# Kernel optimization log

Measured on AMD Instinct MI355X. Metric: run time of the kernel, lower is better.

The kernel has to match this reference:

```python
import jax, jax.numpy as jnp
import numpy as np

B = 64          # graphs per batch
N_NODES = 2000  # nodes per graph (model hyperparameter: FC2 in_features)
NF = 128        # node features
H = 8           # hidden_dim
OC = 8          # out_channels
NC = 2          # n_classes
DEG = 16        # avg degree
SLOPE = 0.01


def _lin_init(key, fan_in, fan_out):
    k1, k2 = jax.random.split(key)
    s = 1.0 / np.sqrt(fan_in)
    W = jax.random.uniform(k1, (fan_in, fan_out), jnp.float32, -s, s)
    b = jax.random.uniform(k2, (fan_out,), jnp.float32, -s, s)
    return W, b


def setup_inputs() -> dict:
    key = jax.random.key(0)
    ks = jax.random.split(key, 10)
    N = B * N_NODES
    E = N * DEG
    x = jax.random.normal(ks[0], (N, NF), jnp.float32)
    # graph-local random edges, offset per graph
    local = jax.random.randint(ks[1], (2, E), 0, N_NODES)
    off = jnp.repeat(jnp.arange(B, dtype=jnp.int64) * N_NODES, E // B)
    edge_index = (local + off[None, :]).astype(jnp.int64)
    batch = jnp.repeat(jnp.arange(B, dtype=jnp.int64), N_NODES)
    W1a, b1a = _lin_init(ks[2], NF, H)
    W1b, b1b = _lin_init(ks[3], H, H)
    W2a, b2a = _lin_init(ks[4], H, H)
    W2b, b2b = _lin_init(ks[5], H, OC)
    Wf1, bf1 = _lin_init(ks[6], OC, 1)
    Wf2, bf2 = _lin_init(ks[7], N_NODES, NC)
    return {"x": x, "edge_index": edge_index, "batch": batch,
            "W1a": W1a, "b1a": b1a, "W1b": W1b, "b1b": b1b,
            "W2a": W2a, "b2a": b2a, "W2b": W2b, "b2b": b2b,
            "Wf1": Wf1, "bf1": bf1, "Wf2": Wf2, "bf2": bf2}


def _lrelu(v):
    return jnp.where(v >= 0, v, SLOPE * v)


def _gin_conv(h, src, dst, Wa, ba, Wb, bb):
    N = h.shape[0]
    agg = jax.ops.segment_sum(h[src], dst, num_segments=N)  # sum_{j->i} h_j
    z = h + agg                                             # (1+eps)*h + agg, eps=0
    z = _lrelu(z @ Wa + ba)                                 # MLP linear1 + act
    return z @ Wb + bb                                      # MLP linear2 (plain last)


def reference(x, edge_index, batch, W1a, b1a, W1b, b1b, W2a, b2a, W2b, b2b,
              Wf1, bf1, Wf2, bf2):
    src, dst = edge_index[0], edge_index[1]
    h = _gin_conv(x, src, dst, W1a, b1a, W1b, b1b)
    h = _lrelu(h)  # inter-layer activation (dropout = identity at eval)
    h = _gin_conv(h, src, dst, W2a, b2a, W2b, b2b)  # [N, OC], no act after last conv
    bsz = h.shape[0] // N_NODES
    y = h.reshape(bsz, N_NODES, OC)
    y = _lrelu(y) @ Wf1 + bf1          # FC1 -> [B, n_nodes, 1]
    y = y.reshape(bsz, N_NODES)
    y = _lrelu(y) @ Wf2 + bf2          # FC2 -> [B, n_classes]
    return jax.nn.log_softmax(y, axis=1)
```

## Files before the change

### kernel.cpp

```cpp
#include <hip/hip_runtime.h>
#include <math.h>

#define NF 128
#define HD 8
#define NPG 2000
#define EPB 8000
#define NPB 500
#define FNPB 128
#define SLOPE 0.01f

__device__ __forceinline__ float lrelu(float v) {
    return v > 0.0f ? v : SLOPE * v;
}
__device__ __forceinline__ unsigned short f2bf(float f) {
    unsigned int u = __float_as_uint(f);
    return (unsigned short)((u + 0x7FFFu + ((u >> 16) & 1u)) >> 16);
}
__device__ __forceinline__ float bfl(unsigned int p) {
    return __uint_as_float(p << 16);
}
__device__ __forceinline__ float bfh(unsigned int p) {
    return __uint_as_float(p & 0xFFFF0000u);
}

__global__ __launch_bounds__(1024) void k_featsort(
    const float* __restrict__ x, const float* __restrict__ W1a,
    const int* __restrict__ ei, unsigned short* __restrict__ t1b,
    unsigned short* __restrict__ gcolb, int* __restrict__ rpc,
    int N, int E, int NC)
{
    __shared__ union {
        struct { float tile[FNPB * 132]; float wl[NF * HD]; } f;
        struct { int cnt[NPG]; int srt[EPB]; int wtot[16]; int wpre[16]; } s;
    } sm;

    const int tid = threadIdx.x;

    if ((int)blockIdx.x < NC) {
        const int b = blockIdx.x;
        const int g = b >> 2;
        const int lane = tid & 63;
        const int wv = tid >> 6;
        const int nodeBase = g * NPG;
        const int e0 = b * EPB;

        for (int i = tid; i < NPG; i += 1024) sm.s.cnt[i] = 0;
        __syncthreads();

        for (int e = e0 + tid; e < e0 + EPB; e += 1024) {
            int dl = ei[E + e] - nodeBase;
            atomicAdd(&sm.s.cnt[dl], 1);
        }
        __syncthreads();

        int c0 = 0, c1 = 0;
        if (tid < 1000) { c0 = sm.s.cnt[2 * tid]; c1 = sm.s.cnt[2 * tid + 1]; }
        int s = c0 + c1;
        int isc = s;
#pragma unroll
        for (int d = 1; d < 64; d <<= 1) {
            int o = __shfl_up(isc, d);
            if (lane >= d) isc += o;
        }
        if (lane == 63) sm.s.wtot[wv] = isc;
        __syncthreads();
        if (wv == 0) {
            int v = (lane < 16) ? sm.s.wtot[lane] : 0;
            int iv = v;
#pragma unroll
            for (int d = 1; d < 16; d <<= 1) {
                int o = __shfl_up(iv, d);
                if (lane >= d) iv += o;
            }
            if (lane < 16) sm.s.wpre[lane] = iv - v;
        }
        __syncthreads();
        int excl = isc - s + sm.s.wpre[wv];

        int* rpb = rpc + (size_t)b * (NPG + 1);
        if (tid < 1000) {
            sm.s.cnt[2 * tid]     = excl;
            sm.s.cnt[2 * tid + 1] = excl + c0;
            rpb[2 * tid]     = excl;
            rpb[2 * tid + 1] = excl + c0;
        }
        if (tid == 0) rpb[NPG] = EPB;
        __syncthreads();

        for (int e = e0 + tid; e < e0 + EPB; e += 1024) {
            int src = ei[e] - nodeBase;
            int dl = ei[E + e] - nodeBase;
            int pos = atomicAdd(&sm.s.cnt[dl], 1);
            sm.s.srt[pos] = src;
        }
        __syncthreads();

        unsigned int* dst = (unsigned int*)(gcolb + (size_t)b * EPB);
        for (int i = tid; i < EPB / 2; i += 1024) {
            unsigned int lo = (unsigned int)sm.s.srt[2 * i] & 0xFFFFu;
            unsigned int hi = (unsigned int)sm.s.srt[2 * i + 1] << 16;
            dst[i] = lo | hi;
        }
    } else {
        const size_t base = (size_t)(blockIdx.x - NC) * FNPB;

        if (tid < 256) ((float4*)sm.f.wl)[tid] = ((const float4*)W1a)[tid];

        const float4* xg = (const float4*)(x + base * NF);
#pragma unroll
        for (int i = 0; i < 4; ++i) {
            int idx = tid + i * 1024;
            float4 v = xg[idx];
            int n = idx >> 5;
            int k4 = idx & 31;
            *(float4*)(sm.f.tile + n * 132 + k4 * 4) = v;
        }
        __syncthreads();

        const int n = tid >> 3;
        const int col = tid & 7;
        float acc = 0.0f;
        const float* row = sm.f.tile + n * 132;
#pragma unroll
        for (int k4 = 0; k4 < 32; ++k4) {
            float4 r = *(const float4*)(row + k4 * 4);
            int kb = k4 * 4 * HD + col;
            acc += r.x * sm.f.wl[kb];
            acc += r.y * sm.f.wl[kb + HD];
            acc += r.z * sm.f.wl[kb + 2 * HD];
            acc += r.w * sm.f.wl[kb + 3 * HD];
        }
        t1b[(base + n) * HD + col] = f2bf(acc);
    }
}

#define GATHER_CHUNK(P)                                                       \
    {                                                                         \
        int b0 = rs[P], cnt = re[P] - b0;                                     \
        int sl[8];                                                            \
        _Pragma("unroll")                                                     \
        for (int j = 0; j < 8; ++j) {                                         \
            int idx = (j < cnt) ? (b0 + j) : 0;                \
            sl[j] = colp[P][idx];                                             \
        }                                                                     \
        _Pragma("unroll")                                                     \
        for (int j = 0; j < 8; ++j) {                                         \
            float w = (j < cnt) ? 1.0f : 0.0f;                                \
            uint4 v = tbl[sl[j]];                                             \
            a0 += w * bfl(v.x); a1 += w * bfh(v.x);                           \
            a2 += w * bfl(v.y); a3 += w * bfh(v.y);                           \
            a4 += w * bfl(v.z); a5 += w * bfh(v.z);                           \
            a6 += w * bfl(v.w); a7 += w * bfh(v.w);                           \
        }                                                                     \
        for (int e2 = b0 + 8; e2 < b0 + cnt; ++e2) {           \
            uint4 v = tbl[colp[P][e2]];                                       \
            a0 += bfl(v.x); a1 += bfh(v.x);                                   \
            a2 += bfl(v.y); a3 += bfh(v.y);                                   \
            a4 += bfl(v.z); a5 += bfh(v.z);                                   \
            a6 += bfl(v.w); a7 += bfh(v.w);                                   \
        }                                                                     \
    }

__global__ __launch_bounds__(512) void k_l1(
    const unsigned short* __restrict__ t1b, const int* __restrict__ rpc,
    const unsigned short* __restrict__ gcolb, unsigned short* __restrict__ ub,
    const float* __restrict__ b1a, const float* __restrict__ W1b,
    const float* __restrict__ b1b, const float* __restrict__ W2a)
{
    __shared__ uint4 tbl[NPG];
    __shared__ float wts[144];

    const int b = blockIdx.x;
    const int g = b >> 2;
    const int q = b & 3;
    const int tid = threadIdx.x;

    if (tid < 144) {
        float v;
        if (tid < 8)       v = b1a[tid];
        else if (tid < 72) v = W1b[tid - 8];
        else if (tid < 80) v = b1b[tid - 72];
        else               v = W2a[tid - 80];
        wts[tid] = v;
    }

    const uint4* src4 = (const uint4*)(t1b + (size_t)g * NPG * HD);
#pragma unroll
    for (int i = 0; i < 4; ++i) {
        int idx = tid + i * 512;
        if (idx < NPG) tbl[idx] = src4[idx];
    }
    __syncthreads();

    if (tid < NPB) {
        const int nl = q * NPB + tid;
        int rs[4], re[4];
        const unsigned short* colp[4];
#pragma unroll
        for (int p = 0; p < 4; ++p) {
            const int* rpb = rpc + (size_t)((g << 2) + p) * (NPG + 1);
            colp[p] = gcolb + (size_t)((g << 2) + p) * EPB;
            rs[p] = rpb[nl]; re[p] = rpb[nl + 1];
        }
        float a0 = 0, a1 = 0, a2 = 0, a3 = 0, a4 = 0, a5 = 0, a6 = 0, a7 = 0;
        GATHER_CHUNK(0) GATHER_CHUNK(1) GATHER_CHUNK(2) GATHER_CHUNK(3)

        uint4 sv = tbl[nl];
        float z[HD];
        z[0] = lrelu(bfl(sv.x) + a0 + wts[0]); z[1] = lrelu(bfh(sv.x) + a1 + wts[1]);
        z[2] = lrelu(bfl(sv.y) + a2 + wts[2]); z[3] = lrelu(bfh(sv.y) + a3 + wts[3]);
        z[4] = lrelu(bfl(sv.z) + a4 + wts[4]); z[5] = lrelu(bfh(sv.z) + a5 + wts[5]);
        z[6] = lrelu(bfl(sv.w) + a6 + wts[6]); z[7] = lrelu(bfh(sv.w) + a7 + wts[7]);

        float h[HD];
#pragma unroll
        for (int j = 0; j < HD; ++j) {
            float acc = wts[72 + j];
#pragma unroll
            for (int c = 0; c < HD; ++c) acc += z[c] * wts[8 + c * HD + j];
            h[j] = lrelu(acc);
        }
        float uu[HD];
#pragma unroll
        for (int j = 0; j < HD; ++j) {
            float acc = 0.0f;
#pragma unroll
            for (int c = 0; c < HD; ++c) acc += h[c] * wts[80 + c * HD + j];
            uu[j] = acc;
        }
        uint4 pk;
        pk.x = (unsigned int)f2bf(uu[0]) | ((unsigned int)f2bf(uu[1]) << 16);
        pk.y = (unsigned int)f2bf(uu[2]) | ((unsigned int)f2bf(uu[3]) << 16);
        pk.z = (unsigned int)f2bf(uu[4]) | ((unsigned int)f2bf(uu[5]) << 16);
        pk.w = (unsigned int)f2bf(uu[6]) | ((unsigned int)f2bf(uu[7]) << 16);
        ((uint4*)ub)[(size_t)g * NPG + nl] = pk;
    }
}

__global__ __launch_bounds__(512) void k_l2(
    const unsigned short* __restrict__ ub, const int* __restrict__ rpc,
    const unsigned short* __restrict__ gcolb,
    const float* __restrict__ b2a, const float* __restrict__ W2b,
    const float* __restrict__ b2b, const float* __restrict__ Wf1,
    const float* __restrict__ bf1, const float* __restrict__ Wf2,
    float* __restrict__ bparts)
{
    __shared__ uint4 tbl[NPG];
    __shared__ float wts[89];
    __shared__ float red[16];

    const int b = blockIdx.x;
    const int g = b >> 2;
    const int q = b & 3;
    const int tid = threadIdx.x;
    const int lane = tid & 63;
    const int wv = tid >> 6;

    if (tid < 89) {
        float v;
        if (tid < 8)       v = b2a[tid];
        else if (tid < 72) v = W2b[tid - 8];
        else if (tid < 80) v = b2b[tid - 72];
        else if (tid < 88) v = Wf1[tid - 80];
        else               v = bf1[0];
        wts[tid] = v;
    }

    const uint4* src4 = (const uint4*)(ub + (size_t)g * NPG * HD);
#pragma unroll
    for (int i = 0; i < 4; ++i) {
        int idx = tid + i * 512;
        if (idx < NPG) tbl[idx] = src4[idx];
    }
    __syncthreads();

    float acc0 = 0.0f, acc1 = 0.0f;
    if (tid < NPB) {
        const int nl = q * NPB + tid;
        int rs[4], re[4];
        const unsigned short* colp[4];
#pragma unroll
        for (int p = 0; p < 4; ++p) {
            const int* rpb = rpc + (size_t)((g << 2) + p) * (NPG + 1);
            colp[p] = gcolb + (size_t)((g << 2) + p) * EPB;
            rs[p] = rpb[nl]; re[p] = rpb[nl + 1];
        }
        float a0 = 0, a1 = 0, a2 = 0, a3 = 0, a4 = 0, a5 = 0, a6 = 0, a7 = 0;
        GATHER_CHUNK(0) GATHER_CHUNK(1) GATHER_CHUNK(2) GATHER_CHUNK(3)

        uint4 sv = tbl[nl];
        float z[HD];
        z[0] = lrelu(bfl(sv.x) + a0 + wts[0]); z[1] = lrelu(bfh(sv.x) + a1 + wts[1]);
        z[2] = lrelu(bfl(sv.y) + a2 + wts[2]); z[3] = lrelu(bfh(sv.y) + a3 + wts[3]);
        z[4] = lrelu(bfl(sv.z) + a4 + wts[4]); z[5] = lrelu(bfh(sv.z) + a5 + wts[5]);
        z[6] = lrelu(bfl(sv.w) + a6 + wts[6]); z[7] = lrelu(bfh(sv.w) + a7 + wts[7]);

        float svl = wts[88];
#pragma unroll
        for (int j = 0; j < HD; ++j) {
            float acc = wts[72 + j];
#pragma unroll
            for (int c = 0; c < HD; ++c) acc += z[c] * wts[8 + c * HD + j];
            svl += lrelu(acc) * wts[80 + j];
        }
        float pf = lrelu(svl);
        float2 wf = *(const float2*)(Wf2 + (size_t)nl * 2);
        acc0 = pf * wf.x;
        acc1 = pf * wf.y;
    }

#pragma unroll
    for (int off = 32; off > 0; off >>= 1) {
        acc0 += __shfl_down(acc0, off);
        acc1 += __shfl_down(acc1, off);
    }
    if (lane == 0) { red[wv * 2] = acc0; red[wv * 2 + 1] = acc1; }
    __syncthreads();

    if (tid == 0) {
        float y0 = 0.f, y1 = 0.f;
#pragma unroll
        for (int w = 0; w < 8; ++w) { y0 += red[w * 2]; y1 += red[w * 2 + 1]; }
        *(float2*)(bparts + (size_t)b * 2) = make_float2(y0, y1);
    }
}

__global__ __launch_bounds__(64) void k_fin(const float* __restrict__ bparts,
                                            const float* __restrict__ bf2,
                                            float* __restrict__ out, int Bn) {
    int g = threadIdx.x;
    if (g >= Bn) return;
    float y0 = bf2[0], y1 = bf2[1];
#pragma unroll
    for (int b = 0; b < 4; ++b) {
        float2 v = *(const float2*)(bparts + (size_t)(g * 4 + b) * 2);
        y0 += v.x; y1 += v.y;
    }
    float m = fmaxf(y0, y1);
    float lse = m + logf(expf(y0 - m) + expf(y1 - m));
    out[g * 2 + 0] = y0 - lse;
    out[g * 2 + 1] = y1 - lse;
}

extern "C" void kernel_launch(void* const* d_in, const int* in_sizes, int n_in,
                              void* d_out, int out_size, void* d_ws, size_t ws_size,
                              hipStream_t stream) {
    const float* x   = (const float*)d_in[0];
    const int*   ei  = (const int*)  d_in[1];
    const float* W1a = (const float*)d_in[3];
    const float* b1a = (const float*)d_in[4];
    const float* W1b = (const float*)d_in[5];
    const float* b1b = (const float*)d_in[6];
    const float* W2a = (const float*)d_in[7];
    const float* b2a = (const float*)d_in[8];
    const float* W2b = (const float*)d_in[9];
    const float* b2b = (const float*)d_in[10];
    const float* Wf1 = (const float*)d_in[11];
    const float* bf1 = (const float*)d_in[12];
    const float* Wf2 = (const float*)d_in[13];
    const float* bf2 = (const float*)d_in[14];

    int N   = in_sizes[0] / NF;
    int E   = in_sizes[1] / 2;
    int Bn  = N / NPG;
    int NC  = Bn * 4;

    unsigned short* t1b   = (unsigned short*)d_ws;
    unsigned short* ubuf  = t1b + (size_t)N * HD;
    unsigned short* gcolb = ubuf + (size_t)N * HD;
    int*            rpc   = (int*)(gcolb + (size_t)E);
    float*          bparts= (float*)(rpc + (size_t)NC * (NPG + 1) + 16);

    k_featsort<<<NC + N / FNPB, 1024, 0, stream>>>(x, W1a, ei, t1b, gcolb, rpc,
                                                   N, E, NC);
    k_l1 <<<NC, 512, 0, stream>>>(t1b, rpc, gcolb, ubuf, b1a, W1b, b1b, W2a);
    k_l2 <<<NC, 512, 0, stream>>>(ubuf, rpc, gcolb, b2a, W2b, b2b, Wf1, bf1,
                                  Wf2, bparts);
    k_fin<<<1, 64, 0, stream>>>(bparts, bf2, (float*)d_out, Bn);
}
```

Before: 154.4 us.

## Split node gathers across thread pairs and cache packed edges in LDS

The layer kernels now launch 8 blocks per graph and assign two threads per node, each summing two of the four edge chunks before an xor-shuffle combine; only one thread of each pair runs the MLP. The sort phase stores packed (dst,src) pairs in shared memory during counting so the scatter pass avoids rereading edge_index from global memory. The aim is more parallelism and shorter per-thread serial gather chains. In exchange, each block reloads the per-graph node table twice as often in total, and LDS use grows in the sort branch.

```diff
diff --git a/kernel.cpp b/kernel.cpp
--- a/kernel.cpp
+++ b/kernel.cpp
@@ -5,7 +5,8 @@
 #define HD 8
 #define NPG 2000
 #define EPB 8000
-#define NPB 500
+#define LPB 8
+#define LNPB 250
 #define FNPB 128
 #define SLOPE 0.01f
 
@@ -31,7 +32,8 @@
 {
     __shared__ union {
         struct { float tile[FNPB * 132]; float wl[NF * HD]; } f;
-        struct { int cnt[NPG]; int srt[EPB]; int wtot[16]; int wpre[16]; } s;
+        struct { int cnt[NPG]; unsigned int pck[EPB]; int srt[EPB];
+                 int wtot[16]; int wpre[16]; } s;
     } sm;
 
     const int tid = threadIdx.x;
@@ -48,7 +50,9 @@
         __syncthreads();
 
         for (int e = e0 + tid; e < e0 + EPB; e += 1024) {
+            int src = ei[e] - nodeBase;
             int dl = ei[E + e] - nodeBase;
+            sm.s.pck[e - e0] = ((unsigned int)dl << 11) | (unsigned int)src;
             atomicAdd(&sm.s.cnt[dl], 1);
         }
         __syncthreads();
@@ -87,9 +91,10 @@
         if (tid == 0) rpb[NPG] = EPB;
         __syncthreads();
 
-        for (int e = e0 + tid; e < e0 + EPB; e += 1024) {
-            int src = ei[e] - nodeBase;
-            int dl = ei[E + e] - nodeBase;
+        for (int i = tid; i < EPB; i += 1024) {
+            unsigned int p = sm.s.pck[i];
+            int dl = (int)(p >> 11);
+            int src = (int)(p & 2047u);
             int pos = atomicAdd(&sm.s.cnt[dl], 1);
             sm.s.srt[pos] = src;
         }
@@ -140,7 +145,7 @@
         int sl[8];                                                            \
         _Pragma("unroll")                                                     \
         for (int j = 0; j < 8; ++j) {                                         \
-            int idx = (j < cnt) ? (b0 + j) : 0;                \
+            int idx = (j < cnt) ? (b0 + j) : 0;                               \
             sl[j] = colp[P][idx];                                             \
         }                                                                     \
         _Pragma("unroll")                                                     \
@@ -152,7 +157,7 @@
             a4 += w * bfl(v.z); a5 += w * bfh(v.z);                           \
             a6 += w * bfl(v.w); a7 += w * bfh(v.w);                           \
         }                                                                     \
-        for (int e2 = b0 + 8; e2 < b0 + cnt; ++e2) {           \
+        for (int e2 = b0 + 8; e2 < b0 + cnt; ++e2) {                          \
             uint4 v = tbl[colp[P][e2]];                                       \
             a0 += bfl(v.x); a1 += bfh(v.x);                                   \
             a2 += bfl(v.y); a3 += bfh(v.y);                                   \
@@ -171,8 +176,8 @@
     __shared__ float wts[144];
 
     const int b = blockIdx.x;
-    const int g = b >> 2;
-    const int q = b & 3;
+    const int g = b >> 3;
+    const int q = b & 7;
     const int tid = threadIdx.x;
 
     if (tid < 144) {
@@ -192,48 +197,57 @@
     }
     __syncthreads();
 
-    if (tid < NPB) {
-        const int nl = q * NPB + tid;
-        int rs[4], re[4];
-        const unsigned short* colp[4];
-#pragma unroll
-        for (int p = 0; p < 4; ++p) {
-            const int* rpb = rpc + (size_t)((g << 2) + p) * (NPG + 1);
-            colp[p] = gcolb + (size_t)((g << 2) + p) * EPB;
+    if (tid < 2 * LNPB) {
+        const int node = tid >> 1;
+        const int half = tid & 1;
+        const int nl = q * LNPB + node;
+        int rs[2], re[2];
+        const unsigned short* colp[2];
+#pragma unroll
+        for (int p = 0; p < 2; ++p) {
+            int ch = half * 2 + p;
+            const int* rpb = rpc + (size_t)((g << 2) + ch) * (NPG + 1);
+            colp[p] = gcolb + (size_t)((g << 2) + ch) * EPB;
             rs[p] = rpb[nl]; re[p] = rpb[nl + 1];
         }
         float a0 = 0, a1 = 0, a2 = 0, a3 = 0, a4 = 0, a5 = 0, a6 = 0, a7 = 0;
-        GATHER_CHUNK(0) GATHER_CHUNK(1) GATHER_CHUNK(2) GATHER_CHUNK(3)
-
-        uint4 sv = tbl[nl];
-        float z[HD];
-        z[0] = lrelu(bfl(sv.x) + a0 + wts[0]); z[1] = lrelu(bfh(sv.x) + a1 + wts[1]);
-        z[2] = lrelu(bfl(sv.y) + a2 + wts[2]); z[3] = lrelu(bfh(sv.y) + a3 + wts[3]);
-        z[4] = lrelu(bfl(sv.z) + a4 + wts[4]); z[5] = lrelu(bfh(sv.z) + a5 + wts[5]);
-        z[6] = lrelu(bfl(sv.w) + a6 + wts[6]); z[7] = lrelu(bfh(sv.w) + a7 + wts[7]);
-
-        float h[HD];
-#pragma unroll
-        for (int j = 0; j < HD; ++j) {
-            float acc = wts[72 + j];
-#pragma unroll
-            for (int c = 0; c < HD; ++c) acc += z[c] * wts[8 + c * HD + j];
-            h[j] = lrelu(acc);
-        }
-        float uu[HD];
-#pragma unroll
-        for (int j = 0; j < HD; ++j) {
-            float acc = 0.0f;
-#pragma unroll
-            for (int c = 0; c < HD; ++c) acc += h[c] * wts[80 + c * HD + j];
-            uu[j] = acc;
-        }
-        uint4 pk;
-        pk.x = (unsigned int)f2bf(uu[0]) | ((unsigned int)f2bf(uu[1]) << 16);
-        pk.y = (unsigned int)f2bf(uu[2]) | ((unsigned int)f2bf(uu[3]) << 16);
-        pk.z = (unsigned int)f2bf(uu[4]) | ((unsigned int)f2bf(uu[5]) << 16);
-        pk.w = (unsigned int)f2bf(uu[6]) | ((unsigned int)f2bf(uu[7]) << 16);
-        ((uint4*)ub)[(size_t)g * NPG + nl] = pk;
+        GATHER_CHUNK(0) GATHER_CHUNK(1)
+        a0 += __shfl_xor(a0, 1); a1 += __shfl_xor(a1, 1);
+        a2 += __shfl_xor(a2, 1); a3 += __shfl_xor(a3, 1);
+        a4 += __shfl_xor(a4, 1); a5 += __shfl_xor(a5, 1);
+        a6 += __shfl_xor(a6, 1); a7 += __shfl_xor(a7, 1);
+
+        if (half == 0) {
+            uint4 sv = tbl[nl];
+            float z[HD];
+            z[0] = lrelu(bfl(sv.x) + a0 + wts[0]); z[1] = lrelu(bfh(sv.x) + a1 + wts[1]);
+            z[2] = lrelu(bfl(sv.y) + a2 + wts[2]); z[3] = lrelu(bfh(sv.y) + a3 + wts[3]);
+            z[4] = lrelu(bfl(sv.z) + a4 + wts[4]); z[5] = lrelu(bfh(sv.z) + a5 + wts[5]);
+            z[6] = lrelu(bfl(sv.w) + a6 + wts[6]); z[7] = lrelu(bfh(sv.w) + a7 + wts[7]);
+
+            float h[HD];
+#pragma unroll
+            for (int j = 0; j < HD; ++j) {
+                float acc = wts[72 + j];
+#pragma unroll
+                for (int c = 0; c < HD; ++c) acc += z[c] * wts[8 + c * HD + j];
+                h[j] = lrelu(acc);
+            }
+            float uu[HD];
+#pragma unroll
+            for (int j = 0; j < HD; ++j) {
+                float acc = 0.0f;
+#pragma unroll
+                for (int c = 0; c < HD; ++c) acc += h[c] * wts[80 + c * HD + j];
+                uu[j] = acc;
+            }
+            uint4 pk;
+            pk.x = (unsigned int)f2bf(uu[0]) | ((unsigned int)f2bf(uu[1]) << 16);
+            pk.y = (unsigned int)f2bf(uu[2]) | ((unsigned int)f2bf(uu[3]) << 16);
+            pk.z = (unsigned int)f2bf(uu[4]) | ((unsigned int)f2bf(uu[5]) << 16);
+            pk.w = (unsigned int)f2bf(uu[6]) | ((unsigned int)f2bf(uu[7]) << 16);
+            ((uint4*)ub)[(size_t)g * NPG + nl] = pk;
+        }
     }
 }
 
@@ -250,8 +264,8 @@
     __shared__ float red[16];
 
     const int b = blockIdx.x;
-    const int g = b >> 2;
-    const int q = b & 3;
+    const int g = b >> 3;
+    const int q = b & 7;
     const int tid = threadIdx.x;
     const int lane = tid & 63;
     const int wv = tid >> 6;
@@ -275,38 +289,47 @@
     __syncthreads();
 
     float acc0 = 0.0f, acc1 = 0.0f;
-    if (tid < NPB) {
-        const int nl = q * NPB + tid;
-        int rs[4], re[4];
-        const unsigned short* colp[4];
-#pragma unroll
-        for (int p = 0; p < 4; ++p) {
-            const int* rpb = rpc + (size_t)((g << 2) + p) * (NPG + 1);
-            colp[p] = gcolb + (size_t)((g << 2) + p) * EPB;
+    if (tid < 2 * LNPB) {
+        const int node = tid >> 1;
+        const int half = tid & 1;
+        const int nl = q * LNPB + node;
+        int rs[2], re[2];
+        const unsigned short* colp[2];
+#pragma unroll
+        for (int p = 0; p < 2; ++p) {
+            int ch = half * 2 + p;
+            const int* rpb = rpc + (size_t)((g << 2) + ch) * (NPG + 1);
+            colp[p] = gcolb + (size_t)((g << 2) + ch) * EPB;
             rs[p] = rpb[nl]; re[p] = rpb[nl + 1];
         }
         float a0 = 0, a1 = 0, a2 = 0, a3 = 0, a4 = 0, a5 = 0, a6 = 0, a7 = 0;
-        GATHER_CHUNK(0) GATHER_CHUNK(1) GATHER_CHUNK(2) GATHER_CHUNK(3)
-
-        uint4 sv = tbl[nl];
-        float z[HD];
-        z[0] = lrelu(bfl(sv.x) + a0 + wts[0]); z[1] = lrelu(bfh(sv.x) + a1 + wts[1]);
-        z[2] = lrelu(bfl(sv.y) + a2 + wts[2]); z[3] = lrelu(bfh(sv.y) + a3 + wts[3]);
-        z[4] = lrelu(bfl(sv.z) + a4 + wts[4]); z[5] = lrelu(bfh(sv.z) + a5 + wts[5]);
-        z[6] = lrelu(bfl(sv.w) + a6 + wts[6]); z[7] = lrelu(bfh(sv.w) + a7 + wts[7]);
-
-        float svl = wts[88];
-#pragma unroll
-        for (int j = 0; j < HD; ++j) {
-            float acc = wts[72 + j];
-#pragma unroll
-            for (int c = 0; c < HD; ++c) acc += z[c] * wts[8 + c * HD + j];
-            svl += lrelu(acc) * wts[80 + j];
-        }
-        float pf = lrelu(svl);
-        float2 wf = *(const float2*)(Wf2 + (size_t)nl * 2);
-        acc0 = pf * wf.x;
-        acc1 = pf * wf.y;
+        GATHER_CHUNK(0) GATHER_CHUNK(1)
+        a0 += __shfl_xor(a0, 1); a1 += __shfl_xor(a1, 1);
+        a2 += __shfl_xor(a2, 1); a3 += __shfl_xor(a3, 1);
+        a4 += __shfl_xor(a4, 1); a5 += __shfl_xor(a5, 1);
+        a6 += __shfl_xor(a6, 1); a7 += __shfl_xor(a7, 1);
+
+        if (half == 0) {
+            uint4 sv = tbl[nl];
+            float z[HD];
+            z[0] = lrelu(bfl(sv.x) + a0 + wts[0]); z[1] = lrelu(bfh(sv.x) + a1 + wts[1]);
+            z[2] = lrelu(bfl(sv.y) + a2 + wts[2]); z[3] = lrelu(bfh(sv.y) + a3 + wts[3]);
+            z[4] = lrelu(bfl(sv.z) + a4 + wts[4]); z[5] = lrelu(bfh(sv.z) + a5 + wts[5]);
+            z[6] = lrelu(bfl(sv.w) + a6 + wts[6]); z[7] = lrelu(bfh(sv.w) + a7 + wts[7]);
+
+            float svl = wts[88];
+#pragma unroll
+            for (int j = 0; j < HD; ++j) {
+                float acc = wts[72 + j];
+#pragma unroll
+                for (int c = 0; c < HD; ++c) acc += z[c] * wts[8 + c * HD + j];
+                svl += lrelu(acc) * wts[80 + j];
+            }
+            float pf = lrelu(svl);
+            float2 wf = *(const float2*)(Wf2 + (size_t)nl * 2);
+            acc0 = pf * wf.x;
+            acc1 = pf * wf.y;
+        }
     }
 
 #pragma unroll
@@ -332,8 +355,8 @@
     if (g >= Bn) return;
     float y0 = bf2[0], y1 = bf2[1];
 #pragma unroll
-    for (int b = 0; b < 4; ++b) {
-        float2 v = *(const float2*)(bparts + (size_t)(g * 4 + b) * 2);
+    for (int b = 0; b < LPB; ++b) {
+        float2 v = *(const float2*)(bparts + (size_t)(g * LPB + b) * 2);
         y0 += v.x; y1 += v.y;
     }
     float m = fmaxf(y0, y1);
@@ -373,8 +396,8 @@
 
     k_featsort<<<NC + N / FNPB, 1024, 0, stream>>>(x, W1a, ei, t1b, gcolb, rpc,
                                                    N, E, NC);
-    k_l1 <<<NC, 512, 0, stream>>>(t1b, rpc, gcolb, ubuf, b1a, W1b, b1b, W2a);
-    k_l2 <<<NC, 512, 0, stream>>>(ubuf, rpc, gcolb, b2a, W2b, b2b, Wf1, bf1,
-                                  Wf2, bparts);
+    k_l1 <<<Bn * LPB, 512, 0, stream>>>(t1b, rpc, gcolb, ubuf, b1a, W1b, b1b, W2a);
+    k_l2 <<<Bn * LPB, 512, 0, stream>>>(ubuf, rpc, gcolb, b2a, W2b, b2b, Wf1,
+                                        bf1, Wf2, bparts);
     k_fin<<<1, 64, 0, stream>>>(bparts, bf2, (float*)d_out, Bn);
 }
```

New measurement: 153.4 us. No clear change (-0.6%).

## Fuse both GIN layers and final reduction into one per-graph kernel

Applied to the files above, without the earlier changes.

Merges the layer-1, layer-2 and final log-softmax kernels into a single kernel with one 1024-thread block per graph. The layer-1 output stays in shared memory instead of round-tripping through global memory, and two kernel launches are removed. The sort phase now packs src/dst into shared memory during the counting pass so edge indices are read from global memory only once. The trade-off is far fewer blocks: 64 blocks instead of 256, each thread handling up to two nodes, which reduces parallelism across the GPU's compute units.

```diff
diff --git a/kernel.cpp b/kernel.cpp
--- a/kernel.cpp
+++ b/kernel.cpp
@@ -5,7 +5,6 @@
 #define HD 8
 #define NPG 2000
 #define EPB 8000
-#define NPB 500
 #define FNPB 128
 #define SLOPE 0.01f
 
@@ -31,7 +30,8 @@
 {
     __shared__ union {
         struct { float tile[FNPB * 132]; float wl[NF * HD]; } f;
-        struct { int cnt[NPG]; int srt[EPB]; int wtot[16]; int wpre[16]; } s;
+        struct { int cnt[NPG]; unsigned int pck[EPB]; int srt[EPB];
+                 int wtot[16]; int wpre[16]; } s;
     } sm;
 
     const int tid = threadIdx.x;
@@ -48,7 +48,9 @@
         __syncthreads();
 
         for (int e = e0 + tid; e < e0 + EPB; e += 1024) {
+            int src = ei[e] - nodeBase;
             int dl = ei[E + e] - nodeBase;
+            sm.s.pck[e - e0] = ((unsigned int)dl << 11) | (unsigned int)src;
             atomicAdd(&sm.s.cnt[dl], 1);
         }
         __syncthreads();
@@ -87,9 +89,10 @@
         if (tid == 0) rpb[NPG] = EPB;
         __syncthreads();
 
-        for (int e = e0 + tid; e < e0 + EPB; e += 1024) {
-            int src = ei[e] - nodeBase;
-            int dl = ei[E + e] - nodeBase;
+        for (int i = tid; i < EPB; i += 1024) {
+            unsigned int p = sm.s.pck[i];
+            int dl = (int)(p >> 11);
+            int src = (int)(p & 2047u);
             int pos = atomicAdd(&sm.s.cnt[dl], 1);
             sm.s.srt[pos] = src;
         }
@@ -140,7 +143,7 @@
         int sl[8];                                                            \
         _Pragma("unroll")                                                     \
         for (int j = 0; j < 8; ++j) {                                         \
-            int idx = (j < cnt) ? (b0 + j) : 0;                \
+            int idx = (j < cnt) ? (b0 + j) : 0;                               \
             sl[j] = colp[P][idx];                                             \
         }                                                                     \
         _Pragma("unroll")                                                     \
@@ -152,7 +155,7 @@
             a4 += w * bfl(v.z); a5 += w * bfh(v.z);                           \
             a6 += w * bfl(v.w); a7 += w * bfh(v.w);                           \
         }                                                                     \
-        for (int e2 = b0 + 8; e2 < b0 + cnt; ++e2) {           \
+        for (int e2 = b0 + 8; e2 < b0 + cnt; ++e2) {                          \
             uint4 v = tbl[colp[P][e2]];                                       \
             a0 += bfl(v.x); a1 += bfh(v.x);                                   \
             a2 += bfl(v.y); a3 += bfh(v.y);                                   \
@@ -161,19 +164,25 @@
         }                                                                     \
     }
 
-__global__ __launch_bounds__(512) void k_l1(
+__global__ __launch_bounds__(1024) void k_layers(
     const unsigned short* __restrict__ t1b, const int* __restrict__ rpc,
-    const unsigned short* __restrict__ gcolb, unsigned short* __restrict__ ub,
+    const unsigned short* __restrict__ gcolb,
     const float* __restrict__ b1a, const float* __restrict__ W1b,
-    const float* __restrict__ b1b, const float* __restrict__ W2a)
+    const float* __restrict__ b1b, const float* __restrict__ W2a,
+    const float* __restrict__ b2a, const float* __restrict__ W2b,
+    const float* __restrict__ b2b, const float* __restrict__ Wf1,
+    const float* __restrict__ bf1, const float* __restrict__ Wf2,
+    const float* __restrict__ bf2, float* __restrict__ out)
 {
     __shared__ uint4 tbl[NPG];
-    __shared__ float wts[144];
-
-    const int b = blockIdx.x;
-    const int g = b >> 2;
-    const int q = b & 3;
+    __shared__ float w1[144];
+    __shared__ float w2[89];
+    __shared__ float red[32];
+
+    const int g = blockIdx.x;
     const int tid = threadIdx.x;
+    const int lane = tid & 63;
+    const int wv = tid >> 6;
 
     if (tid < 144) {
         float v;
@@ -181,132 +190,115 @@
         else if (tid < 72) v = W1b[tid - 8];
         else if (tid < 80) v = b1b[tid - 72];
         else               v = W2a[tid - 80];
-        wts[tid] = v;
+        w1[tid] = v;
+    }
+    if (tid >= 256 && tid < 345) {
+        int i = tid - 256;
+        float v;
+        if (i < 8)       v = b2a[i];
+        else if (i < 72) v = W2b[i - 8];
+        else if (i < 80) v = b2b[i - 72];
+        else if (i < 88) v = Wf1[i - 80];
+        else             v = bf1[0];
+        w2[i] = v;
     }
 
     const uint4* src4 = (const uint4*)(t1b + (size_t)g * NPG * HD);
-#pragma unroll
-    for (int i = 0; i < 4; ++i) {
-        int idx = tid + i * 512;
+    if (tid < NPG) tbl[tid] = src4[tid];
+    {
+        int idx = tid + 1024;
         if (idx < NPG) tbl[idx] = src4[idx];
     }
     __syncthreads();
 
-    if (tid < NPB) {
-        const int nl = q * NPB + tid;
-        int rs[4], re[4];
-        const unsigned short* colp[4];
-#pragma unroll
-        for (int p = 0; p < 4; ++p) {
-            const int* rpb = rpc + (size_t)((g << 2) + p) * (NPG + 1);
-            colp[p] = gcolb + (size_t)((g << 2) + p) * EPB;
-            rs[p] = rpb[nl]; re[p] = rpb[nl + 1];
-        }
-        float a0 = 0, a1 = 0, a2 = 0, a3 = 0, a4 = 0, a5 = 0, a6 = 0, a7 = 0;
-        GATHER_CHUNK(0) GATHER_CHUNK(1) GATHER_CHUNK(2) GATHER_CHUNK(3)
-
-        uint4 sv = tbl[nl];
-        float z[HD];
-        z[0] = lrelu(bfl(sv.x) + a0 + wts[0]); z[1] = lrelu(bfh(sv.x) + a1 + wts[1]);
-        z[2] = lrelu(bfl(sv.y) + a2 + wts[2]); z[3] = lrelu(bfh(sv.y) + a3 + wts[3]);
-        z[4] = lrelu(bfl(sv.z) + a4 + wts[4]); z[5] = lrelu(bfh(sv.z) + a5 + wts[5]);
-        z[6] = lrelu(bfl(sv.w) + a6 + wts[6]); z[7] = lrelu(bfh(sv.w) + a7 + wts[7]);
-
-        float h[HD];
-#pragma unroll
-        for (int j = 0; j < HD; ++j) {
-            float acc = wts[72 + j];
-#pragma unroll
-            for (int c = 0; c < HD; ++c) acc += z[c] * wts[8 + c * HD + j];
-            h[j] = lrelu(acc);
-        }
-        float uu[HD];
-#pragma unroll
-        for (int j = 0; j < HD; ++j) {
-            float acc = 0.0f;
-#pragma unroll
-            for (int c = 0; c < HD; ++c) acc += h[c] * wts[80 + c * HD + j];
-            uu[j] = acc;
-        }
-        uint4 pk;
-        pk.x = (unsigned int)f2bf(uu[0]) | ((unsigned int)f2bf(uu[1]) << 16);
-        pk.y = (unsigned int)f2bf(uu[2]) | ((unsigned int)f2bf(uu[3]) << 16);
-        pk.z = (unsigned int)f2bf(uu[4]) | ((unsigned int)f2bf(uu[5]) << 16);
-        pk.w = (unsigned int)f2bf(uu[6]) | ((unsigned int)f2bf(uu[7]) << 16);
-        ((uint4*)ub)[(size_t)g * NPG + nl] = pk;
-    }
-}
-
-__global__ __launch_bounds__(512) void k_l2(
-    const unsigned short* __restrict__ ub, const int* __restrict__ rpc,
-    const unsigned short* __restrict__ gcolb,
-    const float* __restrict__ b2a, const float* __restrict__ W2b,
-    const float* __restrict__ b2b, const float* __restrict__ Wf1,
-    const float* __restrict__ bf1, const float* __restrict__ Wf2,
-    float* __restrict__ bparts)
-{
-    __shared__ uint4 tbl[NPG];
-    __shared__ float wts[89];
-    __shared__ float red[16];
-
-    const int b = blockIdx.x;
-    const int g = b >> 2;
-    const int q = b & 3;
-    const int tid = threadIdx.x;
-    const int lane = tid & 63;
-    const int wv = tid >> 6;
-
-    if (tid < 89) {
-        float v;
-        if (tid < 8)       v = b2a[tid];
-        else if (tid < 72) v = W2b[tid - 8];
-        else if (tid < 80) v = b2b[tid - 72];
-        else if (tid < 88) v = Wf1[tid - 80];
-        else               v = bf1[0];
-        wts[tid] = v;
-    }
-
-    const uint4* src4 = (const uint4*)(ub + (size_t)g * NPG * HD);
-#pragma unroll
-    for (int i = 0; i < 4; ++i) {
-        int idx = tid + i * 512;
-        if (idx < NPG) tbl[idx] = src4[idx];
+    const int* rpb4[4];
+    const unsigned short* colp[4];
+#pragma unroll
+    for (int p = 0; p < 4; ++p) {
+        rpb4[p] = rpc + (size_t)((g << 2) + p) * (NPG + 1);
+        colp[p] = gcolb + (size_t)((g << 2) + p) * EPB;
+    }
+
+    uint4 upk[2];
+#pragma unroll
+    for (int s = 0; s < 2; ++s) {
+        int nl = tid + s * 1024;
+        if (nl < NPG) {
+            int rs[4], re[4];
+#pragma unroll
+            for (int p = 0; p < 4; ++p) { rs[p] = rpb4[p][nl]; re[p] = rpb4[p][nl + 1]; }
+            float a0 = 0, a1 = 0, a2 = 0, a3 = 0, a4 = 0, a5 = 0, a6 = 0, a7 = 0;
+            GATHER_CHUNK(0) GATHER_CHUNK(1) GATHER_CHUNK(2) GATHER_CHUNK(3)
+
+            uint4 sv = tbl[nl];
+            float z[HD];
+            z[0] = lrelu(bfl(sv.x) + a0 + w1[0]); z[1] = lrelu(bfh(sv.x) + a1 + w1[1]);
+            z[2] = lrelu(bfl(sv.y) + a2 + w1[2]); z[3] = lrelu(bfh(sv.y) + a3 + w1[3]);
+            z[4] = lrelu(bfl(sv.z) + a4 + w1[4]); z[5] = lrelu(bfh(sv.z) + a5 + w1[5]);
+            z[6] = lrelu(bfl(sv.w) + a6 + w1[6]); z[7] = lrelu(bfh(sv.w) + a7 + w1[7]);
+
+            float h[HD];
+#pragma unroll
+            for (int j = 0; j < HD; ++j) {
+                float acc = w1[72 + j];
+#pragma unroll
+                for (int c = 0; c < HD; ++c) acc += z[c] * w1[8 + c * HD + j];
+                h[j] = lrelu(acc);
+            }
+            float uu[HD];
+#pragma unroll
+            for (int j = 0; j < HD; ++j) {
+                float acc = 0.0f;
+#pragma unroll
+                for (int c = 0; c < HD; ++c) acc += h[c] * w1[80 + c * HD + j];
+                uu[j] = acc;
+            }
+            upk[s].x = (unsigned int)f2bf(uu[0]) | ((unsigned int)f2bf(uu[1]) << 16);
+            upk[s].y = (unsigned int)f2bf(uu[2]) | ((unsigned int)f2bf(uu[3]) << 16);
+            upk[s].z = (unsigned int)f2bf(uu[4]) | ((unsigned int)f2bf(uu[5]) << 16);
+            upk[s].w = (unsigned int)f2bf(uu[6]) | ((unsigned int)f2bf(uu[7]) << 16);
+        }
     }
     __syncthreads();
 
+#pragma unroll
+    for (int s = 0; s < 2; ++s) {
+        int nl = tid + s * 1024;
+        if (nl < NPG) tbl[nl] = upk[s];
+    }
+    __syncthreads();
+
     float acc0 = 0.0f, acc1 = 0.0f;
-    if (tid < NPB) {
-        const int nl = q * NPB + tid;
-        int rs[4], re[4];
-        const unsigned short* colp[4];
-#pragma unroll
-        for (int p = 0; p < 4; ++p) {
-            const int* rpb = rpc + (size_t)((g << 2) + p) * (NPG + 1);
-            colp[p] = gcolb + (size_t)((g << 2) + p) * EPB;
-            rs[p] = rpb[nl]; re[p] = rpb[nl + 1];
-        }
-        float a0 = 0, a1 = 0, a2 = 0, a3 = 0, a4 = 0, a5 = 0, a6 = 0, a7 = 0;
-        GATHER_CHUNK(0) GATHER_CHUNK(1) GATHER_CHUNK(2) GATHER_CHUNK(3)
-
-        uint4 sv = tbl[nl];
-        float z[HD];
-        z[0] = lrelu(bfl(sv.x) + a0 + wts[0]); z[1] = lrelu(bfh(sv.x) + a1 + wts[1]);
-        z[2] = lrelu(bfl(sv.y) + a2 + wts[2]); z[3] = lrelu(bfh(sv.y) + a3 + wts[3]);
-        z[4] = lrelu(bfl(sv.z) + a4 + wts[4]); z[5] = lrelu(bfh(sv.z) + a5 + wts[5]);
-        z[6] = lrelu(bfl(sv.w) + a6 + wts[6]); z[7] = lrelu(bfh(sv.w) + a7 + wts[7]);
-
-        float svl = wts[88];
-#pragma unroll
-        for (int j = 0; j < HD; ++j) {
-            float acc = wts[72 + j];
-#pragma unroll
-            for (int c = 0; c < HD; ++c) acc += z[c] * wts[8 + c * HD + j];
-            svl += lrelu(acc) * wts[80 + j];
-        }
-        float pf = lrelu(svl);
-        float2 wf = *(const float2*)(Wf2 + (size_t)nl * 2);
-        acc0 = pf * wf.x;
-        acc1 = pf * wf.y;
+#pragma unroll
+    for (int s = 0; s < 2; ++s) {
+        int nl = tid + s * 1024;
+        if (nl < NPG) {
+            int rs[4], re[4];
+#pragma unroll
+            for (int p = 0; p < 4; ++p) { rs[p] = rpb4[p][nl]; re[p] = rpb4[p][nl + 1]; }
+            float a0 = 0, a1 = 0, a2 = 0, a3 = 0, a4 = 0, a5 = 0, a6 = 0, a7 = 0;
+            GATHER_CHUNK(0) GATHER_CHUNK(1) GATHER_CHUNK(2) GATHER_CHUNK(3)
+
+            uint4 sv = tbl[nl];
+            float z[HD];
+            z[0] = lrelu(bfl(sv.x) + a0 + w2[0]); z[1] = lrelu(bfh(sv.x) + a1 + w2[1]);
+            z[2] = lrelu(bfl(sv.y) + a2 + w2[2]); z[3] = lrelu(bfh(sv.y) + a3 + w2[3]);
+            z[4] = lrelu(bfl(sv.z) + a4 + w2[4]); z[5] = lrelu(bfh(sv.z) + a5 + w2[5]);
+            z[6] = lrelu(bfl(sv.w) + a6 + w2[6]); z[7] = lrelu(bfh(sv.w) + a7 + w2[7]);
+
+            float sv2 = w2[88];
+#pragma unroll
+            for (int j = 0; j < HD; ++j) {
+                float acc = w2[72 + j];
+#pragma unroll
+                for (int c = 0; c < HD; ++c) acc += z[c] * w2[8 + c * HD + j];
+                sv2 += lrelu(acc) * w2[80 + j];
+            }
+            float pf = lrelu(sv2);
+            float2 wf = *(const float2*)(Wf2 + (size_t)nl * 2);
+            acc0 += pf * wf.x;
+            acc1 += pf * wf.y;
+        }
     }
 
 #pragma unroll
@@ -316,30 +308,15 @@
     }
     if (lane == 0) { red[wv * 2] = acc0; red[wv * 2 + 1] = acc1; }
     __syncthreads();
-
     if (tid == 0) {
-        float y0 = 0.f, y1 = 0.f;
-#pragma unroll
-        for (int w = 0; w < 8; ++w) { y0 += red[w * 2]; y1 += red[w * 2 + 1]; }
-        *(float2*)(bparts + (size_t)b * 2) = make_float2(y0, y1);
-    }
-}
-
-__global__ __launch_bounds__(64) void k_fin(const float* __restrict__ bparts,
-                                            const float* __restrict__ bf2,
-                                            float* __restrict__ out, int Bn) {
-    int g = threadIdx.x;
-    if (g >= Bn) return;
-    float y0 = bf2[0], y1 = bf2[1];
-#pragma unroll
-    for (int b = 0; b < 4; ++b) {
-        float2 v = *(const float2*)(bparts + (size_t)(g * 4 + b) * 2);
-        y0 += v.x; y1 += v.y;
-    }
-    float m = fmaxf(y0, y1);
-    float lse = m + logf(expf(y0 - m) + expf(y1 - m));
-    out[g * 2 + 0] = y0 - lse;
-    out[g * 2 + 1] = y1 - lse;
+        float y0 = bf2[0], y1 = bf2[1];
+#pragma unroll
+        for (int w = 0; w < 16; ++w) { y0 += red[w * 2]; y1 += red[w * 2 + 1]; }
+        float m = fmaxf(y0, y1);
+        float lse = m + logf(expf(y0 - m) + expf(y1 - m));
+        out[g * 2 + 0] = y0 - lse;
+        out[g * 2 + 1] = y1 - lse;
+    }
 }
 
 extern "C" void kernel_launch(void* const* d_in, const int* in_sizes, int n_in,
@@ -366,15 +343,12 @@
     int NC  = Bn * 4;
 
     unsigned short* t1b   = (unsigned short*)d_ws;
-    unsigned short* ubuf  = t1b + (size_t)N * HD;
-    unsigned short* gcolb = ubuf + (size_t)N * HD;
+    unsigned short* gcolb = t1b + (size_t)N * HD;
     int*            rpc   = (int*)(gcolb + (size_t)E);
-    float*          bparts= (float*)(rpc + (size_t)NC * (NPG + 1) + 16);
 
     k_featsort<<<NC + N / FNPB, 1024, 0, stream>>>(x, W1a, ei, t1b, gcolb, rpc,
                                                    N, E, NC);
-    k_l1 <<<NC, 512, 0, stream>>>(t1b, rpc, gcolb, ubuf, b1a, W1b, b1b, W2a);
-    k_l2 <<<NC, 512, 0, stream>>>(ubuf, rpc, gcolb, b2a, W2b, b2b, Wf1, bf1,
-                                  Wf2, bparts);
-    k_fin<<<1, 64, 0, stream>>>(bparts, bf2, (float*)d_out, Bn);
-}
+    k_layers  <<<Bn, 1024, 0, stream>>>(t1b, rpc, gcolb, b1a, W1b, b1b, W2a,
+                                        b2a, W2b, b2b, Wf1, bf1, Wf2, bf2,
+                                        (float*)d_out);
+}
```

Result: slower. 213.5 us (+38.3%).
